# Kernel optimization log

Measured on AMD Instinct MI355X. Metric: run time of the kernel, lower is better.

The kernel has to match this reference:

```python
import jax, jax.numpy as jnp
import numpy as np

HID = 96
HEADS = 4
SPATIAL = HEADS * 7  # 3h (points) + h (dist) + 3h (direction)
EPS_LN = 1e-5


def layer_norm(x, g, b):
    m = jnp.mean(x, axis=-1, keepdims=True)
    v = jnp.mean(jnp.square(x - m), axis=-1, keepdims=True)
    return (x - m) * jax.lax.rsqrt(v + EPS_LN) * g + b


def build_frames(pos_CA, pos_CB):
    # Vectorized version of _build_frames: per-residue orthonormal frame from CB-CA,
    # identity for the last residue index and for degenerate (near-zero) vectors.
    B, N, _ = pos_CA.shape
    e1 = pos_CB - pos_CA                                   # [B,N,3]
    n1 = jnp.linalg.norm(e1, axis=-1, keepdims=True)
    valid1 = (n1 > 1e-6)[..., 0]
    e1n = e1 / jnp.maximum(n1, 1e-12)
    z_axis = jnp.array([0.0, 0.0, 1.0], dtype=pos_CA.dtype)
    y_axis = jnp.array([0.0, 1.0, 0.0], dtype=pos_CA.dtype)
    e2a = jnp.cross(e1n, jnp.broadcast_to(z_axis, e1n.shape))
    n2a = jnp.linalg.norm(e2a, axis=-1, keepdims=True)
    e2b = jnp.cross(e1n, jnp.broadcast_to(y_axis, e1n.shape))
    use_y = n2a < 1e-6
    e2 = jnp.where(use_y, e2b, e2a)
    n2 = jnp.linalg.norm(e2, axis=-1, keepdims=True)
    valid2 = (n2 > 1e-6)[..., 0]
    e2n = e2 / jnp.maximum(n2, 1e-12)
    e3 = jnp.cross(e1n, e2n)
    frame = jnp.stack([e1n, e2n, e3], axis=-1)             # columns e1,e2,e3 -> [B,N,3,3]
    not_last = (jnp.arange(N) < N - 1)[None, :]            # last residue keeps identity
    valid = (valid1 & valid2 & not_last)[..., None, None]
    eye = jnp.broadcast_to(jnp.eye(3, dtype=pos_CA.dtype), frame.shape)
    return jnp.where(valid, frame, eye)


def setup_inputs() -> dict:
    key = jax.random.key(0)
    ks = jax.random.split(key, 16)
    B, N, H = 2, 2048, HID
    residue_features = jax.random.normal(ks[0], (B, N, H), jnp.float32)
    pos_CA = jax.random.normal(ks[1], (B, N, 3), jnp.float32) * 10.0
    pos_CB = pos_CA + jax.random.normal(ks[2], (B, N, 3), jnp.float32)
    mask = jnp.ones((B, N), dtype=bool)
    s = 1.0 / np.sqrt(H)
    so = 1.0 / np.sqrt(H + SPATIAL)
    return {
        "residue_features": residue_features,
        "pos_CA": pos_CA,
        "pos_CB": pos_CB,
        "mask": mask,
        "Wq": jax.random.normal(ks[3], (H, H), jnp.float32) * s,
        "bq": jax.random.normal(ks[4], (H,), jnp.float32) * 0.01,
        "Wk": jax.random.normal(ks[5], (H, H), jnp.float32) * s,
        "bk": jax.random.normal(ks[6], (H,), jnp.float32) * 0.01,
        "Wv": jax.random.normal(ks[7], (H, H), jnp.float32) * s,
        "bv": jax.random.normal(ks[8], (H,), jnp.float32) * 0.01,
        "Wo": jax.random.normal(ks[9], (H + SPATIAL, H), jnp.float32) * so,
        "bo": jax.random.normal(ks[10], (H,), jnp.float32) * 0.01,
        "g1": jnp.ones((H,), jnp.float32),
        "b1": jnp.zeros((H,), jnp.float32),
        "g2": jnp.ones((H,), jnp.float32),
        "b2": jnp.zeros((H,), jnp.float32),
    }


def reference(residue_features, pos_CA, pos_CB, mask,
              Wq, bq, Wk, bk, Wv, bv, Wo, bo, g1, b1, g2, b2):
    B, N, H = residue_features.shape
    dh = H // HEADS
    frames = build_frames(pos_CA, pos_CB)                       # [B,N,3,3]
    q = (residue_features @ Wq + bq).reshape(B, N, HEADS, dh)
    k = (residue_features @ Wk + bk).reshape(B, N, HEADS, dh)
    v = (residue_features @ Wv + bv).reshape(B, N, HEADS, dh)
    logits = jnp.einsum('blhd,bkhd->blkh', q, k)                # [B,N,N,h]
    m2 = (mask[:, :, None] & mask[:, None, :])[..., None]
    logits = jnp.where(m2, logits, -jnp.inf)
    alpha = jax.nn.softmax(logits, axis=2)                      # softmax over k
    feat_node = jnp.einsum('blkh,bkhd->blhd', alpha, v).reshape(B, N, H)
    rel_pos = pos_CB[:, :, None, :] - pos_CA[:, None, :, :]     # [B,N,N,3]
    bias = jnp.einsum('blkh,blkd->blhd', alpha, rel_pos)        # [B,N,h,3]
    dist = jnp.linalg.norm(bias, axis=-1, keepdims=True)        # [B,N,h,1]
    pts = jnp.einsum('blij,blhj->blhi', frames, bias)           # [B,N,h,3]
    dirn = pts / (jnp.linalg.norm(pts, axis=-1, keepdims=True) + 1e-10)
    feat_spatial = jnp.concatenate(
        [pts.reshape(B, N, -1), dist.reshape(B, N, -1), dirn.reshape(B, N, -1)], axis=-1)
    feat_all = jnp.concatenate([feat_node, feat_spatial], axis=-1)
    h = jax.nn.relu(layer_norm(feat_all @ Wo + bo, g1, b1))
    h = jnp.where(mask[..., None], h, jnp.zeros_like(h))
    return layer_norm(residue_features + h, g2, b2)
```

## Files before the change

kernel.cpp:

```cpp
#include <hip/hip_runtime.h>

#define HID 96
#define NHEADS 4
#define FEAT 124
#define EPS_LN 1e-5f
#define NROWS 4096
#define NB 2048
#define NSPLIT 16

typedef __attribute__((ext_vector_type(8))) short bf16x8;
typedef __attribute__((ext_vector_type(4))) float f32x4;
typedef __attribute__((ext_vector_type(2))) unsigned int uint2v;

__device__ __forceinline__ unsigned short f2bf(float x) {
    unsigned int u = __float_as_uint(x);
    unsigned int r = (u + 0x7FFFu + ((u >> 16) & 1u)) >> 16;
    return (unsigned short)r;
}
__device__ __forceinline__ float bf2f(unsigned short h) {
    return __uint_as_float(((unsigned int)h) << 16);
}

__global__ __launch_bounds__(64) void wpack_kernel(
    const float* __restrict__ Wq, const float* __restrict__ Wk,
    const float* __restrict__ Wv, unsigned short* __restrict__ wf)
{
    int bid = blockIdx.x;
    int mat = bid / 18, kc = (bid / 6) % 3, jt = bid % 6;
    int lane = threadIdx.x;
    const float* W = (mat == 0) ? Wq : (mat == 1) ? Wk : Wv;
    int j = jt * 16 + (lane & 15);
    int t0 = kc * 32 + (lane >> 4) * 8;
    bf16x8 hi, lo;
    #pragma unroll
    for (int e = 0; e < 8; ++e) {
        float v = W[(t0 + e) * HID + j];
        unsigned short h = f2bf(v);
        hi[e] = (short)h;
        lo[e] = (short)f2bf(v - bf2f(h));
    }
    *(bf16x8*)(wf + ((size_t)(bid * 2 + 0) * 64 + lane) * 8) = hi;
    *(bf16x8*)(wf + ((size_t)(bid * 2 + 1) * 64 + lane) * 8) = lo;
}

__global__ __launch_bounds__(64) void qkvfrag_kernel(
    const float* __restrict__ x, const float* __restrict__ pos_CA,
    const float* __restrict__ bq, const float* __restrict__ bk,
    const float* __restrict__ bv, const unsigned short* __restrict__ wf,
    unsigned short* __restrict__ khi, unsigned short* __restrict__ klo,
    unsigned short* __restrict__ qhi, unsigned short* __restrict__ qlo,
    unsigned short* __restrict__ vfr)
{
    int nt = blockIdx.x / 3, mat = blockIdx.x % 3;
    int lane = threadIdx.x;
    int row0 = nt * 16;
    int b = row0 >> 11;
    int ntb = nt & 127;
    int T = ntb >> 1;
    __shared__ float xs[16][97];
    for (int i = lane; i < 16 * HID; i += 64)
        xs[i / HID][i % HID] = x[(size_t)row0 * HID + i];
    __syncthreads();

    int n = lane & 15, g = lane >> 4;
    bf16x8 xh[3], xl[3];
    #pragma unroll
    for (int kc = 0; kc < 3; ++kc)
        #pragma unroll
        for (int e = 0; e < 8; ++e) {
            float v = xs[n][kc * 32 + g * 8 + e];
            unsigned short h = f2bf(v);
            xh[kc][e] = (short)h;
            xl[kc][e] = (short)f2bf(v - bf2f(h));
        }

    const float* bias = (mat == 0) ? bq : (mat == 1) ? bk : bv;

    #pragma unroll
    for (int jt = 0; jt < 6; ++jt) {
        f32x4 acc;
        #pragma unroll
        for (int r = 0; r < 4; ++r) acc[r] = bias[jt * 16 + 4 * g + r];
        #pragma unroll
        for (int kc = 0; kc < 3; ++kc) {
            const unsigned short* A = wf + (size_t)(((mat * 3 + kc) * 6 + jt) * 2) * 512;
            bf16x8 ah = *(const bf16x8*)(A + lane * 8);
            bf16x8 al = *(const bf16x8*)(A + 512 + lane * 8);
            acc = __builtin_amdgcn_mfma_f32_16x16x32_bf16(ah, xh[kc], acc, 0, 0, 0);
            acc = __builtin_amdgcn_mfma_f32_16x16x32_bf16(al, xh[kc], acc, 0, 0, 0);
            acc = __builtin_amdgcn_mfma_f32_16x16x32_bf16(ah, xl[kc], acc, 0, 0, 0);
        }
        if (mat < 2) {
            unsigned short* hi_arr = (mat == 0) ? qhi : khi;
            unsigned short* lo_arr = (mat == 0) ? qlo : klo;
            int jg0 = jt * 16 + 4 * g;
            int h = jg0 / 24;
            int d0 = jg0 - 24 * h;
            int bh = b * NHEADS + h;
            size_t base = ((size_t)(bh * 128 + ntb) * 64 + n + 16 * (d0 >> 3)) * 8 + (d0 & 7);
            unsigned short h0 = f2bf(acc[0]), h1 = f2bf(acc[1]);
            unsigned short h2 = f2bf(acc[2]), h3 = f2bf(acc[3]);
            uint2v hv = { (unsigned int)h0 | ((unsigned int)h1 << 16),
                          (unsigned int)h2 | ((unsigned int)h3 << 16) };
            unsigned short l0 = f2bf(acc[0] - bf2f(h0)), l1 = f2bf(acc[1] - bf2f(h1));
            unsigned short l2 = f2bf(acc[2] - bf2f(h2)), l3 = f2bf(acc[3] - bf2f(h3));
            uint2v lv = { (unsigned int)l0 | ((unsigned int)l1 << 16),
                          (unsigned int)l2 | ((unsigned int)l3 << 16) };
            *(uint2v*)(hi_arr + base) = hv;
            *(uint2v*)(lo_arr + base) = lv;
        } else {
            int g2 = (ntb & 1) * 2 + (n >> 3);
            #pragma unroll
            for (int r = 0; r < 4; ++r) {
                int jg = jt * 16 + 4 * g + r;
                int h = jg / 24;
                int d = jg - 24 * h;
                int bh = b * NHEADS + h;
                size_t vidx = (((size_t)(bh * 64 + T) * 2 + (d >> 4)) * 64
                               + (d & 15) + 16 * g2) * 8 + (n & 7);
                vfr[vidx] = f2bf(acc[r]);
            }
        }
    }

    if (mat == 2) {
        {
            int h = g;
            int bh = b * NHEADS + h;
            size_t fi = ((size_t)(bh * 128 + ntb) * 64 + 48 + n) * 8;
            bf16x8 zz = {0, 0, 0, 0, 0, 0, 0, 0};
            *(bf16x8*)(khi + fi) = zz;
            *(bf16x8*)(klo + fi) = zz;
            *(bf16x8*)(qhi + fi) = zz;
            *(bf16x8*)(qlo + fi) = zz;
        }
        if (lane < 4) {
            int col = 14 + (lane & 1);
            int g2 = (ntb & 1) * 2 + (lane >> 1);
            bf16x8 zz = {0, 0, 0, 0, 0, 0, 0, 0};
            #pragma unroll
            for (int h = 0; h < NHEADS; ++h) {
                int bh = b * NHEADS + h;
                *(bf16x8*)(vfr + (((size_t)(bh * 64 + T) * 2 + 1) * 64 + col + 16 * g2) * 8) = zz;
            }
        }
        {
            int row = row0 + n;
            int h = g;
            int bh = b * NHEADS + h;
            int g2 = (ntb & 1) * 2 + (n >> 3);
            #pragma unroll
            for (int rem = 0; rem < 6; ++rem) {
                int c = rem % 3;
                bool ishi = rem < 3;
                float val = pos_CA[(size_t)row * 3 + c];
                unsigned short hv = f2bf(val);
                unsigned short sv = ishi ? hv : f2bf(val - bf2f(hv));
                int col = (ishi ? 8 : 11) + c;
                vfr[(((size_t)(bh * 64 + T) * 2 + 1) * 64 + col + 16 * g2) * 8 + (n & 7)] = sv;
            }
        }
    }
}

__global__ __launch_bounds__(256) void attn_mfma_kernel(
    const unsigned short* __restrict__ khi, const unsigned short* __restrict__ klo,
    const unsigned short* __restrict__ qhi, const unsigned short* __restrict__ qlo,
    const unsigned short* __restrict__ vfr,
    float* __restrict__ part)
{
    __shared__ unsigned short pfrag[4][2][2][64][8];
    int wid = threadIdx.x >> 6;
    int lane = threadIdx.x & 63;
    int task = blockIdx.x * 4 + wid;
    int qtp = task & 63;
    int bh = (task >> 6) & 7;
    int ks = task >> 9;
    int qcol = lane & 15, g = lane >> 4;

    bf16x8 qh2[2], ql2[2];
    #pragma unroll
    for (int qi2 = 0; qi2 < 2; ++qi2) {
        int qt = qtp * 2 + qi2;
        qh2[qi2] = *(const bf16x8*)(qhi + ((size_t)(bh * 128 + qt) * 64 + lane) * 8);
        ql2[qi2] = *(const bf16x8*)(qlo + ((size_t)(bh * 128 + qt) * 64 + lane) * 8);
    }

    f32x4 z = {0.f, 0.f, 0.f, 0.f};
    f32x4 acc[2][2] = {{z, z}, {z, z}};
    float ll[2] = {0.f, 0.f};

    #pragma unroll
    for (int t8 = 0; t8 < 32 / NSPLIT; ++t8) {
        int kt0 = ks * (128 / NSPLIT) + t8 * 4;
        const unsigned short* kb = khi + ((size_t)(bh * 128 + kt0) * 64 + lane) * 8;
        const unsigned short* lb = klo + ((size_t)(bh * 128 + kt0) * 64 + lane) * 8;
        bf16x8 kh[4], kl[4];
        #pragma unroll
        for (int i = 0; i < 4; ++i) {
            kh[i] = *(const bf16x8*)(kb + i * 512);
            kl[i] = *(const bf16x8*)(lb + i * 512);
        }
        int T0 = ks * (64 / NSPLIT) + t8 * 2;
        const unsigned short* vb = vfr + ((size_t)(bh * 64 + T0) * 2 * 64 + lane) * 8;
        bf16x8 v00 = *(const bf16x8*)(vb);
        bf16x8 v01 = *(const bf16x8*)(vb + 512);
        bf16x8 v10 = *(const bf16x8*)(vb + 1024);
        bf16x8 v11 = *(const bf16x8*)(vb + 1536);

        #pragma unroll
        for (int qi2 = 0; qi2 < 2; ++qi2) {
            f32x4 s[4];
            #pragma unroll
            for (int i = 0; i < 4; ++i) {
                s[i] = __builtin_amdgcn_mfma_f32_16x16x32_bf16(kh[i], qh2[qi2], z, 0, 0, 0);
                s[i] = __builtin_amdgcn_mfma_f32_16x16x32_bf16(kh[i], ql2[qi2], s[i], 0, 0, 0);
                s[i] = __builtin_amdgcn_mfma_f32_16x16x32_bf16(kl[i], qh2[qi2], s[i], 0, 0, 0);
            }
            float p[4][4];
            float ts = 0.f;
            #pragma unroll
            for (int i = 0; i < 4; ++i)
                #pragma unroll
                for (int r = 0; r < 4; ++r) {
                    float pv = __expf(s[i][r]);
                    p[i][r] = pv;
                    ts += pv;
                }
            ts += __shfl_xor(ts, 16, 64);
            ts += __shfl_xor(ts, 32, 64);
            ll[qi2] += ts;

            #pragma unroll
            for (int t = 0; t < 4; ++t) {
                int lp = qcol + 16 * (2 * (t & 1) + (g >> 1));
                unsigned int w0 = (unsigned int)f2bf(p[t][0]) | ((unsigned int)f2bf(p[t][1]) << 16);
                unsigned int w1 = (unsigned int)f2bf(p[t][2]) | ((unsigned int)f2bf(p[t][3]) << 16);
                unsigned int* dst = (unsigned int*)&pfrag[wid][qi2][t >> 1][lp][(g & 1) * 4];
                dst[0] = w0; dst[1] = w1;
            }
            bf16x8 pf0 = *(const bf16x8*)&pfrag[wid][qi2][0][lane][0];
            bf16x8 pf1 = *(const bf16x8*)&pfrag[wid][qi2][1][lane][0];

            acc[qi2][0] = __builtin_amdgcn_mfma_f32_16x16x32_bf16(v00, pf0, acc[qi2][0], 0, 0, 0);
            acc[qi2][0] = __builtin_amdgcn_mfma_f32_16x16x32_bf16(v10, pf1, acc[qi2][0], 0, 0, 0);
            acc[qi2][1] = __builtin_amdgcn_mfma_f32_16x16x32_bf16(v01, pf0, acc[qi2][1], 0, 0, 0);
            acc[qi2][1] = __builtin_amdgcn_mfma_f32_16x16x32_bf16(v11, pf1, acc[qi2][1], 0, 0, 0);
        }
    }

    #pragma unroll
    for (int qi2 = 0; qi2 < 2; ++qi2) {
        int qt = qtp * 2 + qi2;
        float* pp = part + ((size_t)((bh * 128 + qt) * NSPLIT + ks) * 16 + qcol) * 32;
        #pragma unroll
        for (int r = 0; r < 4; ++r) pp[g * 4 + r] = acc[qi2][0][r];
        if (g < 3) {
            #pragma unroll
            for (int r = 0; r < 4; ++r) pp[16 + g * 4 + r] = acc[qi2][1][r];
        } else {
            pp[28] = acc[qi2][1][0];
            pp[29] = acc[qi2][1][1];
            pp[30] = ll[qi2];
        }
    }
}

__global__ __launch_bounds__(128) void finalize_kernel(
    const float* __restrict__ part,
    const float* __restrict__ pos_CA, const float* __restrict__ pos_CB,
    const float* __restrict__ x,
    const float* __restrict__ Wo, const float* __restrict__ bo,
    const float* __restrict__ g1, const float* __restrict__ b1,
    const float* __restrict__ g2, const float* __restrict__ b2,
    float* __restrict__ out)
{
    int row0 = blockIdx.x * 2;
    int tid = threadIdx.x;
    __shared__ float fsL[2][FEAT];
    __shared__ float cawS[2][NHEADS][3];
    __shared__ float st[2][2][2];

    #pragma unroll
    for (int it = 0; it < 2; ++it) {
        int T = tid + it * 128;
        if (T < 240) {
            int r = T / 120, u = T % 120;
            int h = u / 30, vd = u % 30;
            int row = row0 + r;
            int b = row >> 11, n = row & (NB - 1);
            int bh = b * NHEADS + h;
            const float* pb = part + ((size_t)((bh * 128 + (n >> 4)) * NSPLIT) * 16 + (n & 15)) * 32;
            float A = 0.f, L = 0.f, A2 = 0.f;
            #pragma unroll 4
            for (int ks = 0; ks < NSPLIT; ++ks) {
                const float* pk = pb + ks * (16 * 32);
                A += pk[vd];
                L += pk[30];
                if (vd >= 24 && vd < 27) A2 += pk[vd + 3];
            }
            if (vd < 24) fsL[r][h * 24 + vd] = A / L;
            else if (vd < 27) cawS[r][h][vd - 24] = (A + A2) / L;
        }
    }
    __syncthreads();

    if (tid >= 96 && tid < 104) {
        int i2 = tid - 96;
        int r = i2 >> 2, h = i2 & 3;
        int row = row0 + r;
        int n = row & (NB - 1);
        float cax = pos_CA[(size_t)row * 3 + 0];
        float cay = pos_CA[(size_t)row * 3 + 1];
        float caz = pos_CA[(size_t)row * 3 + 2];
        float cbx = pos_CB[(size_t)row * 3 + 0];
        float cby = pos_CB[(size_t)row * 3 + 1];
        float cbz = pos_CB[(size_t)row * 3 + 2];
        float e1x = cbx - cax, e1y = cby - cay, e1z = cbz - caz;
        float n1 = sqrtf(e1x * e1x + e1y * e1y + e1z * e1z);
        bool valid1 = n1 > 1e-6f;
        float inv1 = 1.f / fmaxf(n1, 1e-12f);
        float ax = e1x * inv1, ay = e1y * inv1, az = e1z * inv1;
        float e2x = ay, e2y = -ax, e2z = 0.f;
        float n2a = sqrtf(e2x * e2x + e2y * e2y);
        if (n2a < 1e-6f) { e2x = -az; e2y = 0.f; e2z = ax; }
        float n2 = sqrtf(e2x * e2x + e2y * e2y + e2z * e2z);
        bool valid2 = n2 > 1e-6f;
        float inv2 = 1.f / fmaxf(n2, 1e-12f);
        float bx = e2x * inv2, by = e2y * inv2, bz = e2z * inv2;
        float cx = ay * bz - az * by;
        float cy = az * bx - ax * bz;
        float cz = ax * by - ay * bx;
        bool valid = valid1 && valid2 && (n < NB - 1);
        float F00, F01, F02, F10, F11, F12, F20, F21, F22;
        if (valid) { F00 = ax; F10 = ay; F20 = az;
                     F01 = bx; F11 = by; F21 = bz;
                     F02 = cx; F12 = cy; F22 = cz; }
        else { F00 = 1.f; F01 = 0.f; F02 = 0.f;
               F10 = 0.f; F11 = 1.f; F12 = 0.f;
               F20 = 0.f; F21 = 0.f; F22 = 1.f; }
        float b0 = cbx - cawS[r][h][0];
        float b1v = cby - cawS[r][h][1];
        float b2v = cbz - cawS[r][h][2];
        float dist = sqrtf(b0 * b0 + b1v * b1v + b2v * b2v);
        float p0 = F00 * b0 + F01 * b1v + F02 * b2v;
        float p1 = F10 * b0 + F11 * b1v + F12 * b2v;
        float p2 = F20 * b0 + F21 * b1v + F22 * b2v;
        float pn = sqrtf(p0 * p0 + p1 * p1 + p2 * p2);
        float invp = 1.f / (pn + 1e-10f);
        fsL[r][HID + h * 3 + 0] = p0;
        fsL[r][HID + h * 3 + 1] = p1;
        fsL[r][HID + h * 3 + 2] = p2;
        fsL[r][HID + 12 + h] = dist;
        fsL[r][HID + 16 + h * 3 + 0] = p0 * invp;
        fsL[r][HID + 16 + h * 3 + 1] = p1 * invp;
        fsL[r][HID + 16 + h * 3 + 2] = p2 * invp;
    }
    __syncthreads();

    float y0 = 0.f, y1 = 0.f;
    if (tid < HID) {
        float bj = bo[tid];
        y0 = bj; y1 = bj;
        #pragma unroll 4
        for (int i = 0; i < FEAT; ++i) {
            float w = Wo[i * HID + tid];
            y0 = fmaf(fsL[0][i], w, y0);
            y1 = fmaf(fsL[1][i], w, y1);
        }
    }

    {
        float s0 = y0, q0 = y0 * y0, s1 = y1, q1 = y1 * y1;
        #pragma unroll
        for (int d = 1; d < 64; d <<= 1) {
            s0 += __shfl_xor(s0, d, 64); q0 += __shfl_xor(q0, d, 64);
            s1 += __shfl_xor(s1, d, 64); q1 += __shfl_xor(q1, d, 64);
        }
        if ((tid & 63) == 0) {
            int w = tid >> 6;
            st[0][w][0] = s0; st[0][w][1] = q0;
            st[1][w][0] = s1; st[1][w][1] = q1;
        }
    }
    __syncthreads();
    float mean0 = (st[0][0][0] + st[0][1][0]) * (1.0f / HID);
    float var0  = (st[0][0][1] + st[0][1][1]) * (1.0f / HID) - mean0 * mean0;
    float mean1 = (st[1][0][0] + st[1][1][0]) * (1.0f / HID);
    float var1  = (st[1][0][1] + st[1][1][1]) * (1.0f / HID) - mean1 * mean1;
    __syncthreads();

    float r0 = 0.f, r1 = 0.f;
    if (tid < HID) {
        float gg = g1[tid], bb = b1[tid];
        float h0 = fmaxf((y0 - mean0) * rsqrtf(var0 + EPS_LN) * gg + bb, 0.f);
        float h1 = fmaxf((y1 - mean1) * rsqrtf(var1 + EPS_LN) * gg + bb, 0.f);
        r0 = x[(size_t)(row0 + 0) * HID + tid] + h0;
        r1 = x[(size_t)(row0 + 1) * HID + tid] + h1;
    }

    {
        float s0 = r0, q0 = r0 * r0, s1 = r1, q1 = r1 * r1;
        #pragma unroll
        for (int d = 1; d < 64; d <<= 1) {
            s0 += __shfl_xor(s0, d, 64); q0 += __shfl_xor(q0, d, 64);
            s1 += __shfl_xor(s1, d, 64); q1 += __shfl_xor(q1, d, 64);
        }
        if ((tid & 63) == 0) {
            int w = tid >> 6;
            st[0][w][0] = s0; st[0][w][1] = q0;
            st[1][w][0] = s1; st[1][w][1] = q1;
        }
    }
    __syncthreads();
    mean0 = (st[0][0][0] + st[0][1][0]) * (1.0f / HID);
    var0  = (st[0][0][1] + st[0][1][1]) * (1.0f / HID) - mean0 * mean0;
    mean1 = (st[1][0][0] + st[1][1][0]) * (1.0f / HID);
    var1  = (st[1][0][1] + st[1][1][1]) * (1.0f / HID) - mean1 * mean1;

    if (tid < HID) {
        out[(size_t)(row0 + 0) * HID + tid] =
            (r0 - mean0) * rsqrtf(var0 + EPS_LN) * g2[tid] + b2[tid];
        out[(size_t)(row0 + 1) * HID + tid] =
            (r1 - mean1) * rsqrtf(var1 + EPS_LN) * g2[tid] + b2[tid];
    }
}

extern "C" void kernel_launch(void* const* d_in, const int* in_sizes, int n_in,
                              void* d_out, int out_size, void* d_ws, size_t ws_size,
                              hipStream_t stream)
{
    const float* x      = (const float*)d_in[0];
    const float* pos_CA = (const float*)d_in[1];
    const float* pos_CB = (const float*)d_in[2];
    const float* Wq = (const float*)d_in[4],  *bq = (const float*)d_in[5];
    const float* Wk = (const float*)d_in[6],  *bk = (const float*)d_in[7];
    const float* Wv = (const float*)d_in[8],  *bv = (const float*)d_in[9];
    const float* Wo = (const float*)d_in[10], *bo = (const float*)d_in[11];
    const float* g1 = (const float*)d_in[12], *b1 = (const float*)d_in[13];
    const float* g2 = (const float*)d_in[14], *b2 = (const float*)d_in[15];
    float* out = (float*)d_out;

    const size_t FR = 524288;
    unsigned short* khi = (unsigned short*)d_ws;
    unsigned short* klo = khi + FR;
    unsigned short* qhi = khi + 2 * FR;
    unsigned short* qlo = khi + 3 * FR;
    unsigned short* vfr = khi + 4 * FR;
    const size_t FRAG_BYTES = 5 * FR * 2;
    float* part = (float*)((char*)d_ws + FRAG_BYTES);
    const size_t PART_BYTES = (size_t)8 * 128 * NSPLIT * 16 * 32 * 4;
    unsigned short* wf = (unsigned short*)((char*)d_ws + FRAG_BYTES + PART_BYTES);

    hipLaunchKernelGGL(wpack_kernel, dim3(54), dim3(64), 0, stream, Wq, Wk, Wv, wf);
    hipLaunchKernelGGL(qkvfrag_kernel, dim3(256 * 3), dim3(64), 0, stream,
                       x, pos_CA, bq, bk, bv, wf, khi, klo, qhi, qlo, vfr);
    int nblocks = (8 * 64 * NSPLIT) / 4;
    hipLaunchKernelGGL(attn_mfma_kernel, dim3(nblocks), dim3(256), 0, stream,
                       khi, klo, qhi, qlo, vfr, part);
    hipLaunchKernelGGL(finalize_kernel, dim3(NROWS / 2), dim3(128), 0, stream,
                       part, pos_CA, pos_CB, x, Wo, bo, g1, b1, g2, b2, out);
}
```

Baseline: 59.33 us.

## Replace split-K partial buffer with atomic accumulation into compact per-row buffer

Each attention split now atomically adds its unnormalized output and softmax denominator into a small per-row, per-head accumulator, instead of writing full partials for every split. The accumulator is zeroed inside the QKV fragment kernel, so no extra launch is needed. The finalize kernel then reads one already-reduced vector per row and head rather than summing 16 partials. This cuts a large write-then-read round trip through global memory, at the cost of many float atomics with 16-way contention per address and a non-deterministic summation order. The denominator goes to slot 31, which a lane group also targets with its last accumulator element, so it relies on that element being zero padding.

```diff
diff --git a/kernel.cpp b/kernel.cpp
--- a/kernel.cpp
+++ b/kernel.cpp
@@ -49,7 +49,7 @@
     const float* __restrict__ bv, const unsigned short* __restrict__ wf,
     unsigned short* __restrict__ khi, unsigned short* __restrict__ klo,
     unsigned short* __restrict__ qhi, unsigned short* __restrict__ qlo,
-    unsigned short* __restrict__ vfr)
+    unsigned short* __restrict__ vfr, float* __restrict__ accum)
 {
     int nt = blockIdx.x / 3, mat = blockIdx.x % 3;
     int lane = threadIdx.x;
@@ -57,6 +57,14 @@
     int b = row0 >> 11;
     int ntb = nt & 127;
     int T = ntb >> 1;
+
+    {
+        int gid = blockIdx.x * 64 + lane;
+        f32x4 zz4 = {0.f, 0.f, 0.f, 0.f};
+        for (int i = gid; i < NROWS * NHEADS * 32 / 4; i += 768 * 64)
+            *(f32x4*)(accum + 4 * (size_t)i) = zz4;
+    }
+
     __shared__ float xs[16][97];
     for (int i = lane; i < 16 * HID; i += 64)
         xs[i / HID][i % HID] = x[(size_t)row0 * HID + i];
@@ -167,7 +175,7 @@
     const unsigned short* __restrict__ khi, const unsigned short* __restrict__ klo,
     const unsigned short* __restrict__ qhi, const unsigned short* __restrict__ qlo,
     const unsigned short* __restrict__ vfr,
-    float* __restrict__ part)
+    float* __restrict__ accum)
 {
     __shared__ unsigned short pfrag[4][2][2][64][8];
     int wid = threadIdx.x >> 6;
@@ -252,22 +260,18 @@
     #pragma unroll
     for (int qi2 = 0; qi2 < 2; ++qi2) {
         int qt = qtp * 2 + qi2;
-        float* pp = part + ((size_t)((bh * 128 + qt) * NSPLIT + ks) * 16 + qcol) * 32;
-        #pragma unroll
-        for (int r = 0; r < 4; ++r) pp[g * 4 + r] = acc[qi2][0][r];
-        if (g < 3) {
-            #pragma unroll
-            for (int r = 0; r < 4; ++r) pp[16 + g * 4 + r] = acc[qi2][1][r];
-        } else {
-            pp[28] = acc[qi2][1][0];
-            pp[29] = acc[qi2][1][1];
-            pp[30] = ll[qi2];
-        }
+        int row = (bh >> 2) * NB + qt * 16 + qcol;
+        float* aa = accum + ((size_t)row * NHEADS + (bh & 3)) * 32;
+        #pragma unroll
+        for (int r = 0; r < 4; ++r) atomicAdd(aa + g * 4 + r, acc[qi2][0][r]);
+        #pragma unroll
+        for (int r = 0; r < 4; ++r) atomicAdd(aa + 16 + g * 4 + r, acc[qi2][1][r]);
+        if (g == 0) atomicAdd(aa + 31, ll[qi2]);
     }
 }
 
 __global__ __launch_bounds__(128) void finalize_kernel(
-    const float* __restrict__ part,
+    const float* __restrict__ accum,
     const float* __restrict__ pos_CA, const float* __restrict__ pos_CB,
     const float* __restrict__ x,
     const float* __restrict__ Wo, const float* __restrict__ bo,
@@ -281,26 +285,20 @@
     __shared__ float cawS[2][NHEADS][3];
     __shared__ float st[2][2][2];
 
-    #pragma unroll
-    for (int it = 0; it < 2; ++it) {
-        int T = tid + it * 128;
-        if (T < 240) {
-            int r = T / 120, u = T % 120;
-            int h = u / 30, vd = u % 30;
-            int row = row0 + r;
-            int b = row >> 11, n = row & (NB - 1);
-            int bh = b * NHEADS + h;
-            const float* pb = part + ((size_t)((bh * 128 + (n >> 4)) * NSPLIT) * 16 + (n & 15)) * 32;
-            float A = 0.f, L = 0.f, A2 = 0.f;
-            #pragma unroll 4
-            for (int ks = 0; ks < NSPLIT; ++ks) {
-                const float* pk = pb + ks * (16 * 32);
-                A += pk[vd];
-                L += pk[30];
-                if (vd >= 24 && vd < 27) A2 += pk[vd + 3];
-            }
-            if (vd < 24) fsL[r][h * 24 + vd] = A / L;
-            else if (vd < 27) cawS[r][h][vd - 24] = (A + A2) / L;
+    {
+        int r = tid >> 6;
+        int rest = tid & 63;
+        int h = rest >> 4, i = rest & 15;
+        int row = row0 + r;
+        const float* A = accum + ((size_t)row * NHEADS + h) * 32;
+        float linv = 1.f / A[31];
+        if (i < 12) {
+            int vd = i * 2;
+            fsL[r][h * 24 + vd]     = A[vd] * linv;
+            fsL[r][h * 24 + vd + 1] = A[vd + 1] * linv;
+        } else if (i < 15) {
+            int c = i - 12;
+            cawS[r][h][c] = (A[24 + c] + A[27 + c]) * linv;
         }
     }
     __syncthreads();
@@ -448,16 +446,16 @@
     unsigned short* qlo = khi + 3 * FR;
     unsigned short* vfr = khi + 4 * FR;
     const size_t FRAG_BYTES = 5 * FR * 2;
-    float* part = (float*)((char*)d_ws + FRAG_BYTES);
-    const size_t PART_BYTES = (size_t)8 * 128 * NSPLIT * 16 * 32 * 4;
-    unsigned short* wf = (unsigned short*)((char*)d_ws + FRAG_BYTES + PART_BYTES);
+    float* accum = (float*)((char*)d_ws + FRAG_BYTES);
+    const size_t ACC_BYTES = (size_t)NROWS * NHEADS * 32 * 4;
+    unsigned short* wf = (unsigned short*)((char*)d_ws + FRAG_BYTES + ACC_BYTES);
 
     hipLaunchKernelGGL(wpack_kernel, dim3(54), dim3(64), 0, stream, Wq, Wk, Wv, wf);
     hipLaunchKernelGGL(qkvfrag_kernel, dim3(256 * 3), dim3(64), 0, stream,
-                       x, pos_CA, bq, bk, bv, wf, khi, klo, qhi, qlo, vfr);
+                       x, pos_CA, bq, bk, bv, wf, khi, klo, qhi, qlo, vfr, accum);
     int nblocks = (8 * 64 * NSPLIT) / 4;
     hipLaunchKernelGGL(attn_mfma_kernel, dim3(nblocks), dim3(256), 0, stream,
-                       khi, klo, qhi, qlo, vfr, part);
+                       khi, klo, qhi, qlo, vfr, accum);
     hipLaunchKernelGGL(finalize_kernel, dim3(NROWS / 2), dim3(128), 0, stream,
-                       part, pos_CA, pos_CB, x, Wo, bo, g1, b1, g2, b2, out);
-}
+                       accum, pos_CA, pos_CB, x, Wo, bo, g1, b1, g2, b2, out);
+}
```

New measurement: 154.7 us. 161% more time.
